# Kernel tuning notes

Measured on AMD Instinct MI355X. Metric: run time of the kernel, lower is better.

## Reference

```python
import jax, jax.numpy as jnp
import numpy as np


def setup_inputs() -> dict:
    key = jax.random.key(0)
    ks = jax.random.split(key, 6)
    B, N, F, H, E = 2, 50000, 64, 32, 800000
    x = jax.random.normal(ks[0], (B, N, F), dtype=jnp.float32)
    edge_index = jax.random.randint(ks[1], (2, E), 0, N, dtype=jnp.int64)
    h_cur = jax.random.normal(ks[2], (B, N, H), dtype=jnp.float32)
    c_cur = jax.random.normal(ks[3], (B, N, H), dtype=jnp.float32)
    W = jax.random.normal(ks[4], (F + H, 4 * H), dtype=jnp.float32) * (1.0 / np.sqrt(F + H))
    b = jax.random.normal(ks[5], (4 * H,), dtype=jnp.float32) * 0.01
    return {"x": x, "edge_index": edge_index, "h_cur": h_cur, "c_cur": c_cur, "W": W, "b": b}


def reference(x, edge_index, h_cur, c_cur, W, b):
    B, N, _ = x.shape
    H = h_cur.shape[-1]

    # --- GCNConv on concatenated [x, h] ---
    combined = jnp.concatenate([x, h_cur], axis=-1)          # [B, N, F+H]
    xw = jnp.einsum('bnf,fg->bng', combined, W)              # [B, N, 4H]

    # add self-loops
    loop = jnp.arange(N, dtype=edge_index.dtype)
    src = jnp.concatenate([edge_index[0], loop])             # [E+N]
    dst = jnp.concatenate([edge_index[1], loop])             # [E+N]

    # symmetric degree normalization: deg over target index (PyG gcn_norm)
    deg = jnp.zeros((N,), dtype=xw.dtype).at[dst].add(1.0)
    dinv = jnp.where(deg > 0, jax.lax.rsqrt(deg), 0.0)
    norm = dinv[src] * dinv[dst]                             # [E+N]

    # gather-scale-scatter aggregation
    msgs = xw[:, src, :] * norm[None, :, None]               # [B, E+N, 4H]
    agg = jnp.zeros((B, N, 4 * H), dtype=xw.dtype).at[:, dst, :].add(msgs)
    conv = agg + b                                           # [B, N, 4H]

    # --- LSTM gating ---
    cc_i, cc_f, cc_o, cc_g = jnp.split(conv, 4, axis=-1)
    i = jax.nn.sigmoid(cc_i)
    f = jax.nn.sigmoid(cc_f)
    o = jax.nn.sigmoid(cc_o)
    g = jnp.tanh(cc_g)
    c_next = f * c_cur + i * g
    h_next = o * jnp.tanh(c_next)
    return h_next, c_next
```

## Files before the change

kernel.cpp:

```cpp
#include <hip/hip_runtime.h>
#include <hip/hip_bf16.h>

constexpr int H_DIM = 32;
constexpr int KPAD  = 104;
constexpr int CAP   = 64;
constexpr int CHK   = 64;
constexpr int EPB   = 2048;

typedef __attribute__((ext_vector_type(8))) short bf16x8;
typedef __attribute__((ext_vector_type(4))) float f32x4;

static __device__ __forceinline__ unsigned short f2bf_bits(float v) {
    __hip_bfloat16 b = __float2bfloat16(v);
    return *reinterpret_cast<unsigned short*>(&b);
}
static __device__ __forceinline__ unsigned pack2(float a, float b) {
    return (unsigned)f2bf_bits(a) | ((unsigned)f2bf_bits(b) << 16);
}
static __device__ __forceinline__ float lo_f(unsigned u) { return __uint_as_float(u << 16); }
static __device__ __forceinline__ float hi_f(unsigned u) { return __uint_as_float(u & 0xffff0000u); }

static __device__ __forceinline__ void fma4p(const uint4 u, float d, float* a)
{
    a[0] = fmaf(lo_f(u.x), d, a[0]);
    a[4] = fmaf(hi_f(u.x), d, a[4]);
    a[1] = fmaf(lo_f(u.y), d, a[1]);
    a[5] = fmaf(hi_f(u.y), d, a[5]);
    a[2] = fmaf(lo_f(u.z), d, a[2]);
    a[6] = fmaf(hi_f(u.z), d, a[6]);
    a[3] = fmaf(lo_f(u.w), d, a[3]);
    a[7] = fmaf(hi_f(u.w), d, a[7]);
}

__global__ __launch_bounds__(256)
void part_convert_kernel(const float* __restrict__ x,
                         const float* __restrict__ h,
                         const int* __restrict__ ei,
                         unsigned* __restrict__ part_buf,
                         unsigned char* __restrict__ hcnt,
                         unsigned* __restrict__ z,
                         int N, int E, int NB)
{
    const int bi = blockIdx.x;
    const int t  = threadIdx.x;
    if (bi < NB) {
        __shared__ unsigned loff[256];
        loff[t] = 0u;
        __syncthreads();
        const int e0 = bi * EPB + t;
        #pragma unroll
        for (int j = 0; j < 8; ++j) {
            int e = e0 + 256 * j;
            if (e < E) {
                int src = ei[e];
                int dst = ei[E + e];
                int p   = dst >> 8;
                unsigned pos = atomicAdd(&loff[p], 1u);
                if (pos < CHK)
                    part_buf[((long)p * NB + bi) * CHK + pos] =
                        (unsigned)src | ((unsigned)(dst & 255) << 16);
            }
        }
        __syncthreads();
        hcnt[bi * 256 + t] = (unsigned char)min(loff[t], (unsigned)CHK);
        return;
    }

    long idx = (long)(bi - NB) * 256 + t;
    if (idx >= (long)N * 24) return;
    int n  = (int)(idx / 24);
    int ku = (int)(idx - (long)n * 24);
    int f0 = 4 * ku;
    float4 a, b;
    if (f0 < 64) {
        a = *reinterpret_cast<const float4*>(x + (long)n * 64 + f0);
        b = *reinterpret_cast<const float4*>(x + ((long)N + n) * 64 + f0);
    } else {
        a = *reinterpret_cast<const float4*>(h + (long)n * 32 + (f0 - 64));
        b = *reinterpret_cast<const float4*>(h + ((long)N + n) * 32 + (f0 - 64));
    }
    uint4 o;
    o.x = pack2(a.x, b.x);
    o.y = pack2(a.y, b.y);
    o.z = pack2(a.z, b.z);
    o.w = pack2(a.w, b.w);
    *reinterpret_cast<uint4*>(z + idx * 4) = o;
}

__global__ __launch_bounds__(256)
void bucket_prep_kernel(const unsigned* __restrict__ part_buf,
                        const unsigned char* __restrict__ hcnt,
                        const float* __restrict__ W,
                        unsigned short* __restrict__ Wt,
                        unsigned* __restrict__ cnt,
                        unsigned short* __restrict__ bucket,
                        int N, int NB, int NPART)
{
    const int t = threadIdx.x;
    if ((int)blockIdx.x >= NPART) {
        int gt = ((int)blockIdx.x - NPART) * 256 + t;
        if (gt < 96 * 128) {
            int k = gt >> 7;
            int n = gt & 127;
            Wt[n * 96 + k] = f2bf_bits(W[gt]);
        }
        return;
    }

    __shared__ unsigned lcnt[256];
    __shared__ __align__(16) unsigned short lbuck[256 * CAP];
    const int p = blockIdx.x;
    lcnt[t] = 0u;
    __syncthreads();

    for (int c = t; c < NB; c += 256) {
        int cc = (int)hcnt[c * 256 + p];
        const unsigned* __restrict__ pb = part_buf + ((long)p * NB + c) * CHK;
        for (int jj = 0; jj < cc; jj += 4) {
            uint4 u4 = *reinterpret_cast<const uint4*>(pb + jj);
            unsigned uu[4] = {u4.x, u4.y, u4.z, u4.w};
            #pragma unroll
            for (int q2 = 0; q2 < 4; ++q2) {
                if (jj + q2 < cc) {
                    unsigned u = uu[q2];
                    int dl = (int)((u >> 16) & 0xFFu);
                    unsigned pos = atomicAdd(&lcnt[dl], 1u);
                    if (pos < CAP) lbuck[dl * CAP + pos] = (unsigned short)(u & 0xFFFFu);
                }
            }
        }
    }
    __syncthreads();

    int n = p * 256 + t;
    if (n < N) cnt[n] = lcnt[t];
    #pragma unroll
    for (int j = 0; j < 8; ++j) {
        int idx = t + 256 * j;
        int row = idx >> 3, c = idx & 7;
        int nn = p * 256 + row;
        if (nn < N)
            *reinterpret_cast<uint4*>(bucket + (long)nn * CAP + 8 * c) =
                *reinterpret_cast<const uint4*>(&lbuck[row * CAP + 8 * c]);
    }
}

__global__ __launch_bounds__(256)
void gather_gemm_kernel(const unsigned* __restrict__ cnt,
                        const unsigned short* __restrict__ bucket,
                        const unsigned* __restrict__ z,
                        const unsigned short* __restrict__ Wt,
                        const float* __restrict__ bias,
                        const float* __restrict__ c_cur,
                        float* __restrict__ out,
                        int N)
{
    __shared__ __align__(16) unsigned short As[16 * KPAD];
    __shared__ float ccs[8][128];
    const int t    = threadIdx.x;
    const int n0   = blockIdx.x * 4;
    const int wv   = t >> 6;
    const int lane = t & 63;
    const int g    = lane >> 5;
    const int w    = lane & 31;
    const unsigned* __restrict__ zw = z + 4 * w;

    {
        const int n    = n0 + wv;
        const bool live = (n < N);
        const int nn   = live ? n : 0;
        const int dn   = live ? min((int)cnt[nn], CAP) : 0;
        const unsigned short* __restrict__ brow = bucket + (long)nn * CAP;

        float acc[8];
        #pragma unroll
        for (int j = 0; j < 8; ++j) acc[j] = 0.f;

        for (int base = 0; base < dn; base += 64) {
            int cnt64 = min(64, dn - base);
            int   s_reg = 0;
            float d_reg = 0.f;
            if (lane < cnt64) {
                s_reg = (int)brow[base + lane];
                d_reg = rsqrtf((float)cnt[s_reg] + 1.f);
            }
            for (int i = 0; i < cnt64; i += 16) {
                unsigned so[8]; float dd[8]; uint4 u[8];
                #pragma unroll
                for (int j = 0; j < 8; ++j) {
                    int ij = i + 2 * j + g;
                    so[j] = (unsigned)__shfl(s_reg, ij) * 96u;
                    dd[j] = __shfl(d_reg, ij);
                    if (ij >= cnt64) dd[j] = 0.f;
                }
                #pragma unroll
                for (int j = 0; j < 8; ++j) {
                    int ij = i + 2 * j + g;
                    u[j] = make_uint4(0u, 0u, 0u, 0u);
                    if (w < 24 && ij < cnt64)
                        u[j] = *reinterpret_cast<const uint4*>(zw + so[j]);
                }
                #pragma unroll
                for (int j = 0; j < 8; ++j) fma4p(u[j], dd[j], acc);
            }
        }

        #pragma unroll
        for (int j = 0; j < 8; ++j) acc[j] += __shfl_xor(acc[j], 32);

        if (live && g == 0 && w < 24) {
            float di  = rsqrtf((float)cnt[nn] + 1.f);
            float di2 = di * di;
            uint4 us = *reinterpret_cast<const uint4*>(zw + (unsigned)nn * 96u);
            float l0 = fmaf(di, acc[0], di2 * lo_f(us.x));
            float l1 = fmaf(di, acc[1], di2 * lo_f(us.y));
            float l2 = fmaf(di, acc[2], di2 * lo_f(us.z));
            float l3 = fmaf(di, acc[3], di2 * lo_f(us.w));
            float h0 = fmaf(di, acc[4], di2 * hi_f(us.x));
            float h1 = fmaf(di, acc[5], di2 * hi_f(us.y));
            float h2 = fmaf(di, acc[6], di2 * hi_f(us.z));
            float h3 = fmaf(di, acc[7], di2 * hi_f(us.w));
            *reinterpret_cast<uint2*>(&As[wv * KPAD + 4 * w]) =
                make_uint2(pack2(l0, l1), pack2(l2, l3));
            *reinterpret_cast<uint2*>(&As[(4 + wv) * KPAD + 4 * w]) =
                make_uint2(pack2(h0, h1), pack2(h2, h3));
        }
    }
    __syncthreads();

    const int m = lane & 15;
    const int q = lane >> 4;

    f32x4 a2[2] = {};
    #pragma unroll
    for (int k0 = 0; k0 < 96; k0 += 32) {
        bf16x8 a = *reinterpret_cast<const bf16x8*>(&As[m * KPAD + k0 + q * 8]);
        #pragma unroll
        for (int ntl = 0; ntl < 2; ++ntl) {
            int ct = 2 * wv + ntl;
            bf16x8 b = *reinterpret_cast<const bf16x8*>(&Wt[(ct * 16 + m) * 96 + k0 + q * 8]);
            a2[ntl] = __builtin_amdgcn_mfma_f32_16x16x32_bf16(a, b, a2[ntl], 0, 0, 0);
        }
    }

    if (lane < 32) {
        #pragma unroll
        for (int ntl = 0; ntl < 2; ++ntl) {
            int col = (2 * wv + ntl) * 16 + m;
            #pragma unroll
            for (int r = 0; r < 4; ++r)
                ccs[q * 4 + r][col] = a2[ntl][r];
        }
    }
    __syncthreads();

    const int row = t >> 5;
    const int l   = t & 31;
    const int b   = row >> 2;
    const int ni  = n0 + (row & 3);
    if (ni < N) {
        float cc0 = ccs[row][l]      + bias[l];
        float cc1 = ccs[row][32 + l] + bias[32 + l];
        float cc2 = ccs[row][64 + l] + bias[64 + l];
        float cc3 = ccs[row][96 + l] + bias[96 + l];
        float ig = 1.f / (1.f + __expf(-cc0));
        float fg = 1.f / (1.f + __expf(-cc1));
        float og = 1.f / (1.f + __expf(-cc2));
        float gg = tanhf(cc3);
        long basei = ((long)b * N + ni) * H_DIM + l;
        float c  = c_cur[basei];
        float cn = fmaf(fg, c, ig * gg);
        out[basei]                       = og * tanhf(cn);
        out[(long)2 * N * H_DIM + basei] = cn;
    }
}

extern "C" void kernel_launch(void* const* d_in, const int* in_sizes, int n_in,
                              void* d_out, int out_size, void* d_ws, size_t ws_size,
                              hipStream_t stream)
{
    const float* x    = (const float*)d_in[0];
    const int*   ei   = (const int*)d_in[1];
    const float* h    = (const float*)d_in[2];
    const float* c    = (const float*)d_in[3];
    const float* W    = (const float*)d_in[4];
    const float* bias = (const float*)d_in[5];

    const int  E  = in_sizes[1] / 2;
    const long BN = (long)in_sizes[2] / H_DIM;
    const int  N  = (int)(BN / 2);
    const int  NP = (N + 255) >> 8;
    const int  NB = (E + EPB - 1) / EPB;

    char* ws = (char*)d_ws;
    unsigned* z = (unsigned*)ws;
    size_t off = (size_t)N * 96 * sizeof(unsigned);
    unsigned* cnt = (unsigned*)(ws + off);   off += (size_t)N * sizeof(unsigned);
    unsigned short* bucket = (unsigned short*)(ws + off); off += (size_t)N * CAP * sizeof(unsigned short);
    unsigned short* Wt = (unsigned short*)(ws + off);     off += 96 * 128 * sizeof(unsigned short);
    off = (off + 255) & ~(size_t)255;
    unsigned* part_buf = (unsigned*)(ws + off); off += (size_t)NP * NB * CHK * sizeof(unsigned);
    unsigned char* hcnt = (unsigned char*)(ws + off); off += (size_t)NB * 256;

    int convGrid = (int)(((long)N * 24 + 255) / 256);
    part_convert_kernel<<<NB + convGrid, 256, 0, stream>>>(
        x, h, ei, part_buf, hcnt, z, N, E, NB);

    bucket_prep_kernel<<<NP + 48, 256, 0, stream>>>(
        part_buf, hcnt, W, Wt, cnt, bucket, N, NB, NP);

    int mGrid = (N + 3) / 4;
    gather_gemm_kernel<<<mGrid, 256, 0, stream>>>(
        cnt, bucket, z, Wt, bias, c, (float*)d_out, N);
}
```

Baseline: 187.9 us.

## Make GEMM per-wave with LDS-staged weights, removing block barriers after gather

Stages the full 128x96 bf16 weight matrix into LDS once per block. Each wave then runs its own 16x16x32 MFMAs over all 8 column tiles for its single node, with A rows taken from a wave-private buffer. This removes the two block-wide __syncthreads and the shared ccs staging. The LSTM gating is applied straight from the MFMA accumulators. In exchange, every block pays an extra weight copy into LDS and uses a larger LDS footprint, and most MFMA rows are redundant because only rows 0/1 carry data.

```diff
diff --git a/kernel.cpp b/kernel.cpp
--- a/kernel.cpp
+++ b/kernel.cpp
@@ -155,21 +155,30 @@
                         float* __restrict__ out,
                         int N)
 {
-    __shared__ __align__(16) unsigned short As[16 * KPAD];
-    __shared__ float ccs[8][128];
+    __shared__ __align__(16) unsigned short WtL[128 * KPAD];
+    __shared__ __align__(16) unsigned short As[4][2 * KPAD];
     const int t    = threadIdx.x;
-    const int n0   = blockIdx.x * 4;
     const int wv   = t >> 6;
     const int lane = t & 63;
     const int g    = lane >> 5;
     const int w    = lane & 31;
     const unsigned* __restrict__ zw = z + 4 * w;
 
+    #pragma unroll
+    for (int j = 0; j < 6; ++j) {
+        int idx = t + 256 * j;
+        int r = idx / 12, c = idx - 12 * r;
+        *reinterpret_cast<uint4*>(&WtL[r * KPAD + 8 * c]) =
+            *reinterpret_cast<const uint4*>(&Wt[r * 96 + 8 * c]);
+    }
+    __syncthreads();
+
+    const int n    = blockIdx.x * 4 + wv;
+    const bool live = (n < N);
+    const int nn   = live ? n : 0;
+
     {
-        const int n    = n0 + wv;
-        const bool live = (n < N);
-        const int nn   = live ? n : 0;
-        const int dn   = live ? min((int)cnt[nn], CAP) : 0;
+        const int dn = live ? min((int)cnt[nn], CAP) : 0;
         const unsigned short* __restrict__ brow = bucket + (long)nn * CAP;
 
         float acc[8];
@@ -208,7 +217,7 @@
         #pragma unroll
         for (int j = 0; j < 8; ++j) acc[j] += __shfl_xor(acc[j], 32);
 
-        if (live && g == 0 && w < 24) {
+        if (g == 0 && w < 24) {
             float di  = rsqrtf((float)cnt[nn] + 1.f);
             float di2 = di * di;
             uint4 us = *reinterpret_cast<const uint4*>(zw + (unsigned)nn * 96u);
@@ -220,58 +229,60 @@
             float h1 = fmaf(di, acc[5], di2 * hi_f(us.y));
             float h2 = fmaf(di, acc[6], di2 * hi_f(us.z));
             float h3 = fmaf(di, acc[7], di2 * hi_f(us.w));
-            *reinterpret_cast<uint2*>(&As[wv * KPAD + 4 * w]) =
+            *reinterpret_cast<uint2*>(&As[wv][4 * w]) =
                 make_uint2(pack2(l0, l1), pack2(l2, l3));
-            *reinterpret_cast<uint2*>(&As[(4 + wv) * KPAD + 4 * w]) =
+            *reinterpret_cast<uint2*>(&As[wv][KPAD + 4 * w]) =
                 make_uint2(pack2(h0, h1), pack2(h2, h3));
         }
     }
-    __syncthreads();
+    asm volatile("s_waitcnt lgkmcnt(0)" ::: "memory");
+    __builtin_amdgcn_sched_barrier(0);
 
     const int m = lane & 15;
     const int q = lane >> 4;
-
-    f32x4 a2[2] = {};
+    const unsigned short* __restrict__ arow = &As[wv][(m & 1) * KPAD];
+
+    f32x4 a8[8] = {};
     #pragma unroll
     for (int k0 = 0; k0 < 96; k0 += 32) {
-        bf16x8 a = *reinterpret_cast<const bf16x8*>(&As[m * KPAD + k0 + q * 8]);
-        #pragma unroll
-        for (int ntl = 0; ntl < 2; ++ntl) {
-            int ct = 2 * wv + ntl;
-            bf16x8 b = *reinterpret_cast<const bf16x8*>(&Wt[(ct * 16 + m) * 96 + k0 + q * 8]);
-            a2[ntl] = __builtin_amdgcn_mfma_f32_16x16x32_bf16(a, b, a2[ntl], 0, 0, 0);
-        }
-    }
-
-    if (lane < 32) {
-        #pragma unroll
-        for (int ntl = 0; ntl < 2; ++ntl) {
-            int col = (2 * wv + ntl) * 16 + m;
-            #pragma unroll
-            for (int r = 0; r < 4; ++r)
-                ccs[q * 4 + r][col] = a2[ntl][r];
-        }
-    }
-    __syncthreads();
-
-    const int row = t >> 5;
-    const int l   = t & 31;
-    const int b   = row >> 2;
-    const int ni  = n0 + (row & 3);
-    if (ni < N) {
-        float cc0 = ccs[row][l]      + bias[l];
-        float cc1 = ccs[row][32 + l] + bias[32 + l];
-        float cc2 = ccs[row][64 + l] + bias[64 + l];
-        float cc3 = ccs[row][96 + l] + bias[96 + l];
-        float ig = 1.f / (1.f + __expf(-cc0));
-        float fg = 1.f / (1.f + __expf(-cc1));
-        float og = 1.f / (1.f + __expf(-cc2));
-        float gg = tanhf(cc3);
-        long basei = ((long)b * N + ni) * H_DIM + l;
-        float c  = c_cur[basei];
-        float cn = fmaf(fg, c, ig * gg);
-        out[basei]                       = og * tanhf(cn);
-        out[(long)2 * N * H_DIM + basei] = cn;
+        bf16x8 a = *reinterpret_cast<const bf16x8*>(arow + k0 + q * 8);
+        #pragma unroll
+        for (int ct = 0; ct < 8; ++ct) {
+            bf16x8 b = *reinterpret_cast<const bf16x8*>(&WtL[(ct * 16 + m) * KPAD + k0 + q * 8]);
+            a8[ct] = __builtin_amdgcn_mfma_f32_16x16x32_bf16(a, b, a8[ct], 0, 0, 0);
+        }
+    }
+
+    if (live && q == 0) {
+        const long co = (long)2 * N * H_DIM;
+        #pragma unroll
+        for (int b = 0; b < 2; ++b) {
+            float ci0 = a8[0][b] + bias[m];
+            float ci1 = a8[1][b] + bias[16 + m];
+            float cf0 = a8[2][b] + bias[32 + m];
+            float cf1 = a8[3][b] + bias[48 + m];
+            float co0 = a8[4][b] + bias[64 + m];
+            float co1 = a8[5][b] + bias[80 + m];
+            float cg0 = a8[6][b] + bias[96 + m];
+            float cg1 = a8[7][b] + bias[112 + m];
+            float ig0 = 1.f / (1.f + __expf(-ci0));
+            float ig1 = 1.f / (1.f + __expf(-ci1));
+            float fg0 = 1.f / (1.f + __expf(-cf0));
+            float fg1 = 1.f / (1.f + __expf(-cf1));
+            float og0 = 1.f / (1.f + __expf(-co0));
+            float og1 = 1.f / (1.f + __expf(-co1));
+            float gg0 = tanhf(cg0);
+            float gg1 = tanhf(cg1);
+            long basei = ((long)b * N + nn) * H_DIM;
+            float c0 = c_cur[basei + m];
+            float c1 = c_cur[basei + 16 + m];
+            float cn0 = fmaf(fg0, c0, ig0 * gg0);
+            float cn1 = fmaf(fg1, c1, ig1 * gg1);
+            out[basei + m]           = og0 * tanhf(cn0);
+            out[basei + 16 + m]      = og1 * tanhf(cn1);
+            out[co + basei + m]      = cn0;
+            out[co + basei + 16 + m] = cn1;
+        }
     }
 }
 
```

Result: slower. 231.2 us (+23.0%).
